# Kernel optimization log

Measured on AMD Instinct MI355X. Metric: run time of the kernel, lower is better.

Reference implementation:

```python
import jax, jax.numpy as jnp
import numpy as np

N, C, HD = 8192, 1024, 128

def setup_inputs() -> dict:
    key = jax.random.key(0)
    ks = jax.random.split(key, 9)
    def xavier(k, fan_in, fan_out):
        lim = float(np.sqrt(6.0 / (fan_in + fan_out)))
        return jax.random.uniform(k, (fan_out, fan_in), jnp.float32, -lim, lim)
    return {
        "x": jax.random.normal(ks[0], (N, C), jnp.float32),
        "Wq": xavier(ks[1], C, HD), "bq": jnp.zeros((HD,), jnp.float32),
        "Wk": xavier(ks[2], C, HD), "bk": jnp.zeros((HD,), jnp.float32),
        "Wv": xavier(ks[3], C, C),  "bv": jnp.zeros((C,), jnp.float32),
        "Wo": xavier(ks[4], C, C),  "bo": jnp.zeros((C,), jnp.float32),
    }

def reference(x, Wq, bq, Wk, bk, Wv, bv, Wo, bo):
    scale = HD ** -0.5
    q = x @ Wq.T + bq          # (N, HD)
    k = x @ Wk.T + bk          # (N, HD)
    v = x @ Wv.T + bv          # (N, C)
    scores = (q @ k.T) * scale # (N, N)
    attn = jax.nn.softmax(scores, axis=-1)
    out = attn @ v             # (N, C)
    return out @ Wo.T + bo
```

## Files before the change

### kernel.cpp

```cpp
#include <hip/hip_runtime.h>

#define NTOK 8192
#define CDIM 1024
#define HDIM 128

typedef __attribute__((ext_vector_type(8))) short short8;
typedef __attribute__((ext_vector_type(4))) float floatx4;
typedef __attribute__((ext_vector_type(16))) float floatx16;

__device__ inline unsigned short f2bf(float f) {
    union { float f; unsigned u; } v; v.f = f;
    unsigned r = v.u + 0x7fffu + ((v.u >> 16) & 1u);
    return (unsigned short)(r >> 16);
}
__device__ inline float bf2f(short s) {
    union { unsigned u; float f; } v;
    v.u = ((unsigned)(unsigned short)s) << 16;
    return v.f;
}
__device__ inline void async16(const unsigned short* g, short* l) {
    __builtin_amdgcn_global_load_lds(
        (const __attribute__((address_space(1))) unsigned*)g,
        (__attribute__((address_space(3))) unsigned*)l, 16, 0, 0);
}

__global__ __launch_bounds__(256) void cast_all(
    const float* __restrict__ x,  const float* __restrict__ Wv,
    const float* __restrict__ Wo, const float* __restrict__ Wq,
    const float* __restrict__ Wk,
    unsigned short* __restrict__ xo, unsigned short* __restrict__ wvo,
    unsigned short* __restrict__ woo, unsigned short* __restrict__ wqo,
    unsigned short* __restrict__ wko)
{
    int b = blockIdx.x;
    const float* in; unsigned short* out; int base;
    if (b < 8192)       { in = x;  out = xo;  base = b; }
    else if (b < 9216)  { in = Wv; out = wvo; base = b - 8192; }
    else if (b < 10240) { in = Wo; out = woo; base = b - 9216; }
    else if (b < 10368) { in = Wq; out = wqo; base = b - 10240; }
    else                { in = Wk; out = wko; base = b - 10368; }
    int i = base * 256 + threadIdx.x;
    float4 v = ((const float4*)in)[i];
    ushort4 o;
    o.x = f2bf(v.x); o.y = f2bf(v.y); o.z = f2bf(v.z); o.w = f2bf(v.w);
    ((ushort4*)out)[i] = o;
}

__global__ __launch_bounds__(256) void gemm_qk(
    const unsigned short* __restrict__ A,
    const unsigned short* __restrict__ Wq, const float* __restrict__ bq,
    const unsigned short* __restrict__ Wk, const float* __restrict__ bk,
    unsigned short* __restrict__ qout, unsigned short* __restrict__ kout, int K)
{
    __shared__ short As[4][64][8];
    __shared__ short Ws[4][64][8];
    const int tid = threadIdx.x;
    const int wave = tid >> 6, lane = tid & 63;
    const int lr = lane & 15, lc = lane >> 4;
    const int m0 = blockIdx.x * 64;
    const int isK = blockIdx.y >> 1;
    const int n0 = (blockIdx.y & 1) * 64;
    const unsigned short* W = isK ? Wk : Wq;
    const float* bias = isK ? bk : bq;

    floatx4 acc[4] = {};
    const int srow = tid >> 2, sch = tid & 3;
    const unsigned short* Ag = A + (long)(m0 + srow) * K + sch * 8;
    const unsigned short* Wg = W + (long)(n0 + srow) * K + sch * 8;

    for (int k0 = 0; k0 < K; k0 += 32) {
        *(short8*)&As[sch][srow][0] = *(const short8*)(Ag + k0);
        *(short8*)&Ws[sch][srow][0] = *(const short8*)(Wg + k0);
        __syncthreads();
        short8 a = *(short8*)&As[lc][wave * 16 + lr][0];
#pragma unroll
        for (int s = 0; s < 4; s++) {
            short8 b = *(short8*)&Ws[lc][s * 16 + lr][0];
            acc[s] = __builtin_amdgcn_mfma_f32_16x16x32_bf16(a, b, acc[s], 0, 0, 0);
        }
        __syncthreads();
    }

#pragma unroll
    for (int s = 0; s < 4; s++) {
        int h = n0 + s * 16 + lr;
        float bv = bias[h];
        int tok0 = m0 + wave * 16 + lc * 4;
#pragma unroll
        for (int r = 0; r < 4; r++) {
            int tok = tok0 + r;
            if (isK)
                kout[(tok >> 5) * 4096 + (h >> 3) * 256 + (tok & 31) * 8 + (h & 7)] =
                    f2bf(acc[s][r] + bv);
            else
                qout[(long)tok * HDIM + h] = f2bf(acc[s][r] + bv);
        }
    }
}

template<int MODE>
__global__ __launch_bounds__(256) void gemm128_nt(
    const unsigned short* __restrict__ A, const unsigned short* __restrict__ W,
    const float* __restrict__ bias, void* __restrict__ out, int M, int N, int K)
{
    __shared__ short As[2][128][4][8];
    __shared__ short Ws[2][128][4][8];
    const int tid = threadIdx.x, wave = tid >> 6, lane = tid & 63;
    const int lr = lane & 15, lc = lane >> 4;
    const int wm = (wave >> 1) * 64, wn = (wave & 1) * 64;
    const int m0 = blockIdx.x * 128, n0 = blockIdx.y * 128;

    floatx4 acc[4][4] = {};

    const int srow = lane >> 2, sch = lane & 3;
    const unsigned short* Ag0 = A + (long)(m0 + wave * 32 + srow) * K + sch * 8;
    const unsigned short* Ag1 = Ag0 + (long)16 * K;
    const unsigned short* Wg0 = W + (long)(n0 + wave * 32 + srow) * K + sch * 8;
    const unsigned short* Wg1 = Wg0 + (long)16 * K;

#define GSTAGE(K0, S)                                        \
    {                                                        \
        async16(Ag0 + (K0), &As[S][wave * 32][0][0]);        \
        async16(Ag1 + (K0), &As[S][wave * 32 + 16][0][0]);   \
        async16(Wg0 + (K0), &Ws[S][wave * 32][0][0]);        \
        async16(Wg1 + (K0), &Ws[S][wave * 32 + 16][0][0]);   \
    }

    GSTAGE(0, 0);
    int s = 0;
    for (int k0 = 0; k0 < K; k0 += 32, s ^= 1) {
        __syncthreads();
        if (k0 + 32 < K) GSTAGE(k0 + 32, s ^ 1);
        short8 af[4], bfg[4];
#pragma unroll
        for (int i = 0; i < 4; i++) af[i]  = *(short8*)&As[s][wm + i * 16 + lr][lc][0];
#pragma unroll
        for (int j = 0; j < 4; j++) bfg[j] = *(short8*)&Ws[s][wn + j * 16 + lr][lc][0];
#pragma unroll
        for (int i = 0; i < 4; i++)
#pragma unroll
            for (int j = 0; j < 4; j++)
                acc[i][j] = __builtin_amdgcn_mfma_f32_16x16x32_bf16(af[i], bfg[j], acc[i][j], 0, 0, 0);
    }
#undef GSTAGE

#pragma unroll
    for (int i = 0; i < 4; i++) {
        int t0 = m0 + wm + i * 16 + lc * 4;
#pragma unroll
        for (int j = 0; j < 4; j++) {
            int c = n0 + wn + j * 16 + lr;
            float bv = bias[c];
            if (MODE == 0) {
                float* o = (float*)out;
#pragma unroll
                for (int r = 0; r < 4; r++) o[(long)(t0 + r) * N + c] = acc[i][j][r] + bv;
            } else {
                unsigned short* o = (unsigned short*)out;
                ushort4 pk;
                pk.x = f2bf(acc[i][j][0] + bv); pk.y = f2bf(acc[i][j][1] + bv);
                pk.z = f2bf(acc[i][j][2] + bv); pk.w = f2bf(acc[i][j][3] + bv);
                long off = (long)(c >> 8) * 2097152 + (t0 >> 5) * 8192 +
                           ((t0 & 31) >> 3) * 2048 + (c & 255) * 8 + (t0 & 7);
                *(ushort4*)&o[off] = pk;
            }
        }
    }
}

__global__ __launch_bounds__(512, 2) void attn_pv(
    const unsigned short* __restrict__ qb, const unsigned short* __restrict__ ksw,
    const unsigned short* __restrict__ vsw,
    unsigned short* __restrict__ Oa, unsigned short* __restrict__ Ob,
    float* __restrict__ la, float* __restrict__ lb)
{
    __shared__ short Ks[3][8192];
    __shared__ short Vs[3][16384];

    const int tid = threadIdx.x, wave = tid >> 6, lane = tid & 63;
    const int l31 = lane & 31, h = lane >> 5;
    const int m0 = blockIdx.x * 256, cblk = blockIdx.y;
    const int mw = m0 + wave * 32;
    const int nt0 = blockIdx.z * 128;
    unsigned short* Op = blockIdx.z ? Ob : Oa;
    float* ls = blockIdx.z ? lb : la;
    const float cexp = (float)(0.08838834764831845 * 1.4426950408889634);

    short8 qf[8];
#pragma unroll
    for (int kk = 0; kk < 8; kk++)
        qf[kk] = *(const short8*)&qb[(mw + l31) * HDIM + kk * 16 + h * 8];

    floatx16 acc[8] = {};
    float ls0 = 0.f, ls1 = 0.f, ls2 = 0.f, ls3 = 0.f;

    const unsigned short* kg0 = ksw + (wave * 2 + 0) * 512 + lane * 8;
    const unsigned short* kg1 = ksw + (wave * 2 + 1) * 512 + lane * 8;
    const unsigned short* vgb = vsw + (long)cblk * 2097152 + lane * 8;
    const unsigned short* vg0 = vgb + (wave * 4 + 0) * 512;
    const unsigned short* vg1 = vgb + (wave * 4 + 1) * 512;
    const unsigned short* vg2 = vgb + (wave * 4 + 2) * 512;
    const unsigned short* vg3 = vgb + (wave * 4 + 3) * 512;

    short* kr = &Ks[0][0];
    short* kw = &Ks[1][0];
    short* k2 = &Ks[2][0];
    short* vr = &Vs[0][0];
    short* vw = &Vs[1][0];
    short* v2 = &Vs[2][0];

#define STAGE(P, KD, VD)                                                \
    {                                                                   \
        long ok_ = (long)(nt0 + 2 * (P)) * 4096;                        \
        long ov_ = (long)(nt0 + 2 * (P)) * 8192;                        \
        async16(kg0 + ok_, (KD) + (wave * 2 + 0) * 512);                \
        async16(kg1 + ok_, (KD) + (wave * 2 + 1) * 512);                \
        async16(vg0 + ov_, (VD) + (wave * 4 + 0) * 512);                \
        async16(vg1 + ov_, (VD) + (wave * 4 + 1) * 512);                \
        async16(vg2 + ov_, (VD) + (wave * 4 + 2) * 512);                \
        async16(vg3 + ov_, (VD) + (wave * 4 + 3) * 512);                \
    }

    STAGE(0, kr, vr);

    for (int ph = 0; ph < 64; ++ph) {
        if (ph + 1 < 64) STAGE(ph + 1, kw, vw);
        __builtin_amdgcn_sched_barrier(0);
        if (ph == 63) asm volatile("s_waitcnt vmcnt(0)" ::: "memory");
        else          asm volatile("s_waitcnt vmcnt(6)" ::: "memory");
        __builtin_amdgcn_sched_barrier(0);
        __builtin_amdgcn_s_barrier();
        __builtin_amdgcn_sched_barrier(0);

        short* kb0 = kr;        short* vb0 = vr;
        short* kb1 = kr + 4096; short* vb1 = vr + 8192;

        floatx16 st0 = {}, st1 = {};
        __builtin_amdgcn_s_setprio(1);
#pragma unroll
        for (int kk = 0; kk < 8; kk++) {
            short8 kf0 = *(short8*)(kb0 + (kk * 2 + h) * 256 + l31 * 8);
            short8 kf1 = *(short8*)(kb1 + (kk * 2 + h) * 256 + l31 * 8);
            st0 = __builtin_amdgcn_mfma_f32_32x32x16_bf16(kf0, qf[kk], st0, 0, 0, 0);
            st1 = __builtin_amdgcn_mfma_f32_32x32x16_bf16(kf1, qf[kk], st1, 0, 0, 0);
        }
        __builtin_amdgcn_s_setprio(0);

#define EXP_PACK(ST, PA0, PA1)                                                      \
        short8 PA0, PA1;                                                            \
        {                                                                           \
            unsigned pk0, pk1, pk2, pk3, pk4, pk5, pk6, pk7;                        \
            float p0, p1;                                                           \
            _Pragma("clang diagnostic push")                                        \
            p0 = __builtin_amdgcn_exp2f(ST[0] * cexp);                              \
            p1 = __builtin_amdgcn_exp2f(ST[1] * cexp);                              \
            ls0 += p0 + p1;                                                         \
            asm("v_cvt_pk_bf16_f32 %0, %1, %2" : "=v"(pk0) : "v"(p0), "v"(p1));     \
            p0 = __builtin_amdgcn_exp2f(ST[2] * cexp);                              \
            p1 = __builtin_amdgcn_exp2f(ST[3] * cexp);                              \
            ls1 += p0 + p1;                                                         \
            asm("v_cvt_pk_bf16_f32 %0, %1, %2" : "=v"(pk1) : "v"(p0), "v"(p1));     \
            p0 = __builtin_amdgcn_exp2f(ST[4] * cexp);                              \
            p1 = __builtin_amdgcn_exp2f(ST[5] * cexp);                              \
            ls2 += p0 + p1;                                                         \
            asm("v_cvt_pk_bf16_f32 %0, %1, %2" : "=v"(pk2) : "v"(p0), "v"(p1));     \
            p0 = __builtin_amdgcn_exp2f(ST[6] * cexp);                              \
            p1 = __builtin_amdgcn_exp2f(ST[7] * cexp);                              \
            ls3 += p0 + p1;                                                         \
            asm("v_cvt_pk_bf16_f32 %0, %1, %2" : "=v"(pk3) : "v"(p0), "v"(p1));     \
            p0 = __builtin_amdgcn_exp2f(ST[8] * cexp);                              \
            p1 = __builtin_amdgcn_exp2f(ST[9] * cexp);                              \
            ls0 += p0 + p1;                                                         \
            asm("v_cvt_pk_bf16_f32 %0, %1, %2" : "=v"(pk4) : "v"(p0), "v"(p1));     \
            p0 = __builtin_amdgcn_exp2f(ST[10] * cexp);                             \
            p1 = __builtin_amdgcn_exp2f(ST[11] * cexp);                             \
            ls1 += p0 + p1;                                                         \
            asm("v_cvt_pk_bf16_f32 %0, %1, %2" : "=v"(pk5) : "v"(p0), "v"(p1));     \
            p0 = __builtin_amdgcn_exp2f(ST[12] * cexp);                             \
            p1 = __builtin_amdgcn_exp2f(ST[13] * cexp);                             \
            ls2 += p0 + p1;                                                         \
            asm("v_cvt_pk_bf16_f32 %0, %1, %2" : "=v"(pk6) : "v"(p0), "v"(p1));     \
            p0 = __builtin_amdgcn_exp2f(ST[14] * cexp);                             \
            p1 = __builtin_amdgcn_exp2f(ST[15] * cexp);                             \
            ls3 += p0 + p1;                                                         \
            asm("v_cvt_pk_bf16_f32 %0, %1, %2" : "=v"(pk7) : "v"(p0), "v"(p1));     \
            _Pragma("clang diagnostic pop")                                         \
            asm("v_permlane32_swap_b32 %0, %1" : "+v"(pk0), "+v"(pk2));             \
            asm("v_permlane32_swap_b32 %0, %1" : "+v"(pk1), "+v"(pk3));             \
            asm("v_permlane32_swap_b32 %0, %1" : "+v"(pk4), "+v"(pk6));             \
            asm("v_permlane32_swap_b32 %0, %1" : "+v"(pk5), "+v"(pk7));             \
            union { unsigned u[4]; short8 s; } up0_, up1_;                          \
            up0_.u[0] = pk0; up0_.u[1] = pk1; up0_.u[2] = pk2; up0_.u[3] = pk3;     \
            up1_.u[0] = pk4; up1_.u[1] = pk5; up1_.u[2] = pk6; up1_.u[3] = pk7;     \
            PA0 = up0_.s; PA1 = up1_.s;                                             \
        }

#define PV(VB, PA0, PA1)                                                            \
        __builtin_amdgcn_s_setprio(1);                                              \
        _Pragma("unroll")                                                           \
        for (int ct = 0; ct < 8; ct++) {                                            \
            short8 bv0 = *(short8*)((VB) + h * 2048 + (ct * 32 + l31) * 8);         \
            short8 bv1 = *(short8*)((VB) + (2 + h) * 2048 + (ct * 32 + l31) * 8);   \
            acc[ct] = __builtin_amdgcn_mfma_f32_32x32x16_bf16(PA0, bv0, acc[ct], 0, 0, 0); \
            acc[ct] = __builtin_amdgcn_mfma_f32_32x32x16_bf16(PA1, bv1, acc[ct], 0, 0, 0); \
        }                                                                           \
        __builtin_amdgcn_s_setprio(0);

        EXP_PACK(st0, pa0_0, pa1_0)
        EXP_PACK(st1, pa0_1, pa1_1)
        PV(vb0, pa0_0, pa1_0)
        PV(vb1, pa0_1, pa1_1)

#undef EXP_PACK
#undef PV

        short* t0p = kr; kr = kw; kw = k2; k2 = t0p;
        short* t1p = vr; vr = vw; vw = v2; v2 = t1p;
    }
#undef STAGE

#pragma unroll
    for (int ct = 0; ct < 8; ct++) {
        int c = cblk * 256 + ct * 32 + l31;
#pragma unroll
        for (int r = 0; r < 16; r++) {
            int q = (r & 3) + 8 * (r >> 2) + 4 * h;
            Op[(long)(mw + q) * CDIM + c] = f2bf(acc[ct][r]);
        }
    }
    if (blockIdx.y == 0) {
        float lsum = (ls0 + ls1) + (ls2 + ls3);
        lsum += __shfl_xor(lsum, 32);
        if (lane < 32) ls[mw + lane] = lsum;
    }
}

__global__ __launch_bounds__(256) void combine_attn(
    const unsigned short* __restrict__ Oa, unsigned short* __restrict__ Ob,
    const float* __restrict__ la, const float* __restrict__ lb)
{
    int i = blockIdx.x * blockDim.x + threadIdx.x;
    int row = i >> 7;
    float inv = 1.0f / (la[row] + lb[row]);
    short8 a = ((const short8*)Oa)[i];
    short8 b = ((const short8*)Ob)[i];
    short8 o;
#pragma unroll
    for (int e = 0; e < 8; e++) o[e] = (short)f2bf((bf2f(a[e]) + bf2f(b[e])) * inv);
    ((short8*)Ob)[i] = o;
}

extern "C" void kernel_launch(void* const* d_in, const int* in_sizes, int n_in,
                              void* d_out, int out_size, void* d_ws, size_t ws_size,
                              hipStream_t stream) {
    const float* x  = (const float*)d_in[0];
    const float* Wq = (const float*)d_in[1];
    const float* bq = (const float*)d_in[2];
    const float* Wk = (const float*)d_in[3];
    const float* bk = (const float*)d_in[4];
    const float* Wv = (const float*)d_in[5];
    const float* bv = (const float*)d_in[6];
    const float* Wo = (const float*)d_in[7];
    const float* bo = (const float*)d_in[8];

    char* ws = (char*)d_ws;
    unsigned short* x_bf   = (unsigned short*)(ws + 0);
    unsigned short* wq_bf  = (unsigned short*)(ws + 16777216);
    unsigned short* wk_bf  = (unsigned short*)(ws + 17039360);
    unsigned short* wv_bf  = (unsigned short*)(ws + 17301504);
    unsigned short* wo_bf  = (unsigned short*)(ws + 19398656);
    unsigned short* q_bf   = (unsigned short*)(ws + 21495808);
    unsigned short* k_swz  = (unsigned short*)(ws + 23592960);
    unsigned short* v_swz  = (unsigned short*)(ws + 25690112);
    unsigned short* attn_bf= (unsigned short*)(ws + 42467328);
    float* lsum_a          = (float*)(ws + 59244544);
    float* lsum_b          = (float*)(ws + 59277312);

    cast_all<<<10496, 256, 0, stream>>>(x, Wv, Wo, Wq, Wk,
                                        x_bf, wv_bf, wo_bf, wq_bf, wk_bf);

    gemm_qk<<<dim3(128, 4), 256, 0, stream>>>(x_bf, wq_bf, bq, wk_bf, bk,
                                              q_bf, k_swz, CDIM);
    gemm128_nt<2><<<dim3(64, 8), 256, 0, stream>>>(x_bf, wv_bf, bv, v_swz, NTOK, CDIM, CDIM);

    attn_pv<<<dim3(32, 4, 2), 512, 0, stream>>>(q_bf, k_swz, v_swz,
                                                x_bf, attn_bf, lsum_a, lsum_b);
    combine_attn<<<4096, 256, 0, stream>>>(x_bf, attn_bf, lsum_a, lsum_b);

    gemm128_nt<0><<<dim3(64, 8), 256, 0, stream>>>(attn_bf, wo_bf, bo, d_out, NTOK, CDIM, CDIM);
}
```

Before: 358.8 us.

## Fuse Q/K/V projections into one GEMM launch with triple-buffered async loads

Replaces the separate small-tile Q/K GEMM and the V GEMM with a single 128x128-tile projection kernel whose grid covers Q, K and all V column blocks. Both the projection and output GEMMs move to a three-stage LDS ring with explicit vmcnt waits and a single barrier per k-step, in place of double buffering with full syncs. The aim is to cut a kernel launch, use the faster tiled path for the Q/K projection, and overlap global loads with MFMA work. In exchange it uses more LDS per block and relies on hand-placed wait counts being correct.

Result: faster. 343.7 us (-4.2%).

```diff
diff --git a/kernel.cpp b/kernel.cpp
--- a/kernel.cpp
+++ b/kernel.cpp
@@ -46,65 +46,108 @@
     ((ushort4*)out)[i] = o;
 }
 
-__global__ __launch_bounds__(256) void gemm_qk(
+__global__ __launch_bounds__(256, 2) void gemm_proj(
     const unsigned short* __restrict__ A,
     const unsigned short* __restrict__ Wq, const float* __restrict__ bq,
     const unsigned short* __restrict__ Wk, const float* __restrict__ bk,
-    unsigned short* __restrict__ qout, unsigned short* __restrict__ kout, int K)
+    const unsigned short* __restrict__ Wv, const float* __restrict__ bv,
+    unsigned short* __restrict__ qout, unsigned short* __restrict__ kout,
+    unsigned short* __restrict__ vout)
 {
-    __shared__ short As[4][64][8];
-    __shared__ short Ws[4][64][8];
-    const int tid = threadIdx.x;
-    const int wave = tid >> 6, lane = tid & 63;
+    __shared__ short As[3][128][4][8];
+    __shared__ short Ws[3][128][4][8];
+    const int tid = threadIdx.x, wave = tid >> 6, lane = tid & 63;
     const int lr = lane & 15, lc = lane >> 4;
-    const int m0 = blockIdx.x * 64;
-    const int isK = blockIdx.y >> 1;
-    const int n0 = (blockIdx.y & 1) * 64;
-    const unsigned short* W = isK ? Wk : Wq;
-    const float* bias = isK ? bk : bq;
-
-    floatx4 acc[4] = {};
-    const int srow = tid >> 2, sch = tid & 3;
-    const unsigned short* Ag = A + (long)(m0 + srow) * K + sch * 8;
-    const unsigned short* Wg = W + (long)(n0 + srow) * K + sch * 8;
-
-    for (int k0 = 0; k0 < K; k0 += 32) {
-        *(short8*)&As[sch][srow][0] = *(const short8*)(Ag + k0);
-        *(short8*)&Ws[sch][srow][0] = *(const short8*)(Wg + k0);
-        __syncthreads();
-        short8 a = *(short8*)&As[lc][wave * 16 + lr][0];
-#pragma unroll
-        for (int s = 0; s < 4; s++) {
-            short8 b = *(short8*)&Ws[lc][s * 16 + lr][0];
-            acc[s] = __builtin_amdgcn_mfma_f32_16x16x32_bf16(a, b, acc[s], 0, 0, 0);
-        }
-        __syncthreads();
-    }
-
-#pragma unroll
-    for (int s = 0; s < 4; s++) {
-        int h = n0 + s * 16 + lr;
-        float bv = bias[h];
-        int tok0 = m0 + wave * 16 + lc * 4;
-#pragma unroll
-        for (int r = 0; r < 4; r++) {
-            int tok = tok0 + r;
-            if (isK)
-                kout[(tok >> 5) * 4096 + (h >> 3) * 256 + (tok & 31) * 8 + (h & 7)] =
-                    f2bf(acc[s][r] + bv);
-            else
-                qout[(long)tok * HDIM + h] = f2bf(acc[s][r] + bv);
-        }
-    }
-}
-
-template<int MODE>
-__global__ __launch_bounds__(256) void gemm128_nt(
+    const int wm = (wave >> 1) * 64, wn = (wave & 1) * 64;
+    const int m0 = blockIdx.x * 128;
+    const int y = blockIdx.y;
+
+    const unsigned short* W; const float* bias; int n0;
+    if (y == 0)      { W = Wq; bias = bq; n0 = 0; }
+    else if (y == 1) { W = Wk; bias = bk; n0 = 0; }
+    else             { W = Wv; bias = bv; n0 = (y - 2) * 128; }
+
+    floatx4 acc[4][4] = {};
+
+    const int srow = lane >> 2, sch = lane & 3;
+    const unsigned short* Ag0 = A + (long)(m0 + wave * 32 + srow) * CDIM + sch * 8;
+    const unsigned short* Ag1 = Ag0 + (long)16 * CDIM;
+    const unsigned short* Wg0 = W + (long)(n0 + wave * 32 + srow) * CDIM + sch * 8;
+    const unsigned short* Wg1 = Wg0 + (long)16 * CDIM;
+
+    short* ar = &As[0][0][0][0]; short* aw = &As[1][0][0][0]; short* a2 = &As[2][0][0][0];
+    short* wr = &Ws[0][0][0][0]; short* ww = &Ws[1][0][0][0]; short* w2 = &Ws[2][0][0][0];
+
+#define GSTAGE(K0, AD, WD) {                          \
+        async16(Ag0 + (K0), (AD) + wave * 1024);      \
+        async16(Ag1 + (K0), (AD) + wave * 1024 + 512);\
+        async16(Wg0 + (K0), (WD) + wave * 1024);      \
+        async16(Wg1 + (K0), (WD) + wave * 1024 + 512); }
+
+    GSTAGE(0, ar, wr);
+    for (int k0 = 0; k0 < CDIM; k0 += 32) {
+        if (k0 + 32 < CDIM) {
+            GSTAGE(k0 + 32, aw, ww);
+            __builtin_amdgcn_sched_barrier(0);
+            asm volatile("s_waitcnt vmcnt(4)" ::: "memory");
+        } else {
+            asm volatile("s_waitcnt vmcnt(0)" ::: "memory");
+        }
+        __builtin_amdgcn_sched_barrier(0);
+        __builtin_amdgcn_s_barrier();
+        __builtin_amdgcn_sched_barrier(0);
+        short8 af[4], bfg[4];
+#pragma unroll
+        for (int i = 0; i < 4; i++) af[i]  = *(short8*)(ar + (wm + i * 16 + lr) * 32 + lc * 8);
+#pragma unroll
+        for (int j = 0; j < 4; j++) bfg[j] = *(short8*)(wr + (wn + j * 16 + lr) * 32 + lc * 8);
+#pragma unroll
+        for (int i = 0; i < 4; i++)
+#pragma unroll
+            for (int j = 0; j < 4; j++)
+                acc[i][j] = __builtin_amdgcn_mfma_f32_16x16x32_bf16(af[i], bfg[j], acc[i][j], 0, 0, 0);
+        short* t;
+        t = ar; ar = aw; aw = a2; a2 = t;
+        t = wr; wr = ww; ww = w2; w2 = t;
+    }
+#undef GSTAGE
+
+#pragma unroll
+    for (int i = 0; i < 4; i++) {
+        int t0 = m0 + wm + i * 16 + lc * 4;
+#pragma unroll
+        for (int j = 0; j < 4; j++) {
+            int c = n0 + wn + j * 16 + lr;
+            float bb = bias[c];
+            if (y == 0) {
+#pragma unroll
+                for (int r = 0; r < 4; r++)
+                    qout[(long)(t0 + r) * HDIM + c] = f2bf(acc[i][j][r] + bb);
+            } else if (y == 1) {
+#pragma unroll
+                for (int r = 0; r < 4; r++) {
+                    int tok = t0 + r;
+                    kout[(tok >> 5) * 4096 + (c >> 3) * 256 + (tok & 31) * 8 + (c & 7)] =
+                        f2bf(acc[i][j][r] + bb);
+                }
+            } else {
+                ushort4 pk;
+                pk.x = f2bf(acc[i][j][0] + bb); pk.y = f2bf(acc[i][j][1] + bb);
+                pk.z = f2bf(acc[i][j][2] + bb); pk.w = f2bf(acc[i][j][3] + bb);
+                long off = (long)(c >> 8) * 2097152 + (t0 >> 5) * 8192 +
+                           ((t0 & 31) >> 3) * 2048 + (c & 255) * 8 + (t0 & 7);
+                *(ushort4*)&vout[off] = pk;
+            }
+        }
+    }
+}
+
+__global__ __launch_bounds__(256, 2) void gemm_out(
     const unsigned short* __restrict__ A, const unsigned short* __restrict__ W,
-    const float* __restrict__ bias, void* __restrict__ out, int M, int N, int K)
+    const float* __restrict__ bias, float* __restrict__ out)
 {
-    __shared__ short As[2][128][4][8];
-    __shared__ short Ws[2][128][4][8];
+    __shared__ short As[3][128][4][8];
+    __shared__ short Ws[3][128][4][8];
     const int tid = threadIdx.x, wave = tid >> 6, lane = tid & 63;
     const int lr = lane & 15, lc = lane >> 4;
     const int wm = (wave >> 1) * 64, wn = (wave & 1) * 64;
@@ -113,34 +156,45 @@
     floatx4 acc[4][4] = {};
 
     const int srow = lane >> 2, sch = lane & 3;
-    const unsigned short* Ag0 = A + (long)(m0 + wave * 32 + srow) * K + sch * 8;
-    const unsigned short* Ag1 = Ag0 + (long)16 * K;
-    const unsigned short* Wg0 = W + (long)(n0 + wave * 32 + srow) * K + sch * 8;
-    const unsigned short* Wg1 = Wg0 + (long)16 * K;
-
-#define GSTAGE(K0, S)                                        \
-    {                                                        \
-        async16(Ag0 + (K0), &As[S][wave * 32][0][0]);        \
-        async16(Ag1 + (K0), &As[S][wave * 32 + 16][0][0]);   \
-        async16(Wg0 + (K0), &Ws[S][wave * 32][0][0]);        \
-        async16(Wg1 + (K0), &Ws[S][wave * 32 + 16][0][0]);   \
-    }
-
-    GSTAGE(0, 0);
-    int s = 0;
-    for (int k0 = 0; k0 < K; k0 += 32, s ^= 1) {
-        __syncthreads();
-        if (k0 + 32 < K) GSTAGE(k0 + 32, s ^ 1);
+    const unsigned short* Ag0 = A + (long)(m0 + wave * 32 + srow) * CDIM + sch * 8;
+    const unsigned short* Ag1 = Ag0 + (long)16 * CDIM;
+    const unsigned short* Wg0 = W + (long)(n0 + wave * 32 + srow) * CDIM + sch * 8;
+    const unsigned short* Wg1 = Wg0 + (long)16 * CDIM;
+
+    short* ar = &As[0][0][0][0]; short* aw = &As[1][0][0][0]; short* a2 = &As[2][0][0][0];
+    short* wr = &Ws[0][0][0][0]; short* ww = &Ws[1][0][0][0]; short* w2 = &Ws[2][0][0][0];
+
+#define GSTAGE(K0, AD, WD) {                          \
+        async16(Ag0 + (K0), (AD) + wave * 1024);      \
+        async16(Ag1 + (K0), (AD) + wave * 1024 + 512);\
+        async16(Wg0 + (K0), (WD) + wave * 1024);      \
+        async16(Wg1 + (K0), (WD) + wave * 1024 + 512); }
+
+    GSTAGE(0, ar, wr);
+    for (int k0 = 0; k0 < CDIM; k0 += 32) {
+        if (k0 + 32 < CDIM) {
+            GSTAGE(k0 + 32, aw, ww);
+            __builtin_amdgcn_sched_barrier(0);
+            asm volatile("s_waitcnt vmcnt(4)" ::: "memory");
+        } else {
+            asm volatile("s_waitcnt vmcnt(0)" ::: "memory");
+        }
+        __builtin_amdgcn_sched_barrier(0);
+        __builtin_amdgcn_s_barrier();
+        __builtin_amdgcn_sched_barrier(0);
         short8 af[4], bfg[4];
 #pragma unroll
-        for (int i = 0; i < 4; i++) af[i]  = *(short8*)&As[s][wm + i * 16 + lr][lc][0];
-#pragma unroll
-        for (int j = 0; j < 4; j++) bfg[j] = *(short8*)&Ws[s][wn + j * 16 + lr][lc][0];
+        for (int i = 0; i < 4; i++) af[i]  = *(short8*)(ar + (wm + i * 16 + lr) * 32 + lc * 8);
+#pragma unroll
+        for (int j = 0; j < 4; j++) bfg[j] = *(short8*)(wr + (wn + j * 16 + lr) * 32 + lc * 8);
 #pragma unroll
         for (int i = 0; i < 4; i++)
 #pragma unroll
             for (int j = 0; j < 4; j++)
                 acc[i][j] = __builtin_amdgcn_mfma_f32_16x16x32_bf16(af[i], bfg[j], acc[i][j], 0, 0, 0);
+        short* t;
+        t = ar; ar = aw; aw = a2; a2 = t;
+        t = wr; wr = ww; ww = w2; w2 = t;
     }
 #undef GSTAGE
 
@@ -150,20 +204,9 @@
 #pragma unroll
         for (int j = 0; j < 4; j++) {
             int c = n0 + wn + j * 16 + lr;
-            float bv = bias[c];
-            if (MODE == 0) {
-                float* o = (float*)out;
-#pragma unroll
-                for (int r = 0; r < 4; r++) o[(long)(t0 + r) * N + c] = acc[i][j][r] + bv;
-            } else {
-                unsigned short* o = (unsigned short*)out;
-                ushort4 pk;
-                pk.x = f2bf(acc[i][j][0] + bv); pk.y = f2bf(acc[i][j][1] + bv);
-                pk.z = f2bf(acc[i][j][2] + bv); pk.w = f2bf(acc[i][j][3] + bv);
-                long off = (long)(c >> 8) * 2097152 + (t0 >> 5) * 8192 +
-                           ((t0 & 31) >> 3) * 2048 + (c & 255) * 8 + (t0 & 7);
-                *(ushort4*)&o[off] = pk;
-            }
+            float bb = bias[c];
+#pragma unroll
+            for (int r = 0; r < 4; r++) out[(long)(t0 + r) * CDIM + c] = acc[i][j][r] + bb;
         }
     }
 }
@@ -251,7 +294,6 @@
         {                                                                           \
             unsigned pk0, pk1, pk2, pk3, pk4, pk5, pk6, pk7;                        \
             float p0, p1;                                                           \
-            _Pragma("clang diagnostic push")                                        \
             p0 = __builtin_amdgcn_exp2f(ST[0] * cexp);                              \
             p1 = __builtin_amdgcn_exp2f(ST[1] * cexp);                              \
             ls0 += p0 + p1;                                                         \
@@ -284,7 +326,6 @@
             p1 = __builtin_amdgcn_exp2f(ST[15] * cexp);                             \
             ls3 += p0 + p1;                                                         \
             asm("v_cvt_pk_bf16_f32 %0, %1, %2" : "=v"(pk7) : "v"(p0), "v"(p1));     \
-            _Pragma("clang diagnostic pop")                                         \
             asm("v_permlane32_swap_b32 %0, %1" : "+v"(pk0), "+v"(pk2));             \
             asm("v_permlane32_swap_b32 %0, %1" : "+v"(pk1), "+v"(pk3));             \
             asm("v_permlane32_swap_b32 %0, %1" : "+v"(pk4), "+v"(pk6));             \
@@ -379,13 +420,12 @@
     cast_all<<<10496, 256, 0, stream>>>(x, Wv, Wo, Wq, Wk,
                                         x_bf, wv_bf, wo_bf, wq_bf, wk_bf);
 
-    gemm_qk<<<dim3(128, 4), 256, 0, stream>>>(x_bf, wq_bf, bq, wk_bf, bk,
-                                              q_bf, k_swz, CDIM);
-    gemm128_nt<2><<<dim3(64, 8), 256, 0, stream>>>(x_bf, wv_bf, bv, v_swz, NTOK, CDIM, CDIM);
+    gemm_proj<<<dim3(64, 10), 256, 0, stream>>>(x_bf, wq_bf, bq, wk_bf, bk, wv_bf, bv,
+                                                q_bf, k_swz, v_swz);
 
     attn_pv<<<dim3(32, 4, 2), 512, 0, stream>>>(q_bf, k_swz, v_swz,
                                                 x_bf, attn_bf, lsum_a, lsum_b);
     combine_attn<<<4096, 256, 0, stream>>>(x_bf, attn_bf, lsum_a, lsum_b);
 
-    gemm128_nt<0><<<dim3(64, 8), 256, 0, stream>>>(attn_bf, wo_bf, bo, d_out, NTOK, CDIM, CDIM);
-}
+    gemm_out<<<dim3(64, 8), 256, 0, stream>>>(attn_bf, wo_bf, bo, (float*)d_out);
+}
```
